# Performance work log

Measured on AMD Instinct MI355X. Metric: run time of the kernel, lower is better.

The kernel has to match this reference:

```python
import jax, jax.numpy as jnp
import numpy as np

N_NODES = 50000
N_EDGES = 800000
B, S, D = 512, 200, 128
H = 8


def setup_inputs() -> dict:
    key = jax.random.key(0)
    ks = iter(jax.random.split(key, 64))
    def nrm(shape, scale=0.05):
        return jax.random.normal(next(ks), shape, dtype=jnp.float32) * scale
    inp = {
        'hist_seq': jax.random.randint(next(ks), (B, S), 0, N_NODES, dtype=jnp.int32),
        'hist_answers': jax.random.randint(next(ks), (B, S), 0, 2, dtype=jnp.int32),
        'new_seq': jax.random.randint(next(ks), (B, S), 0, N_NODES, dtype=jnp.int32),
        'edge_index': jax.random.randint(next(ks), (2, N_EDGES), 0, N_NODES, dtype=jnp.int32),
        'node_x': nrm((N_NODES, D)),
        'gcn_w0': nrm((D, D)), 'gcn_b0': jnp.zeros((D,), jnp.float32),
        'gcn_w1': nrm((D, D)), 'gcn_b1': jnp.zeros((D,), jnp.float32),
        'gcn_w2': nrm((D, D)), 'gcn_b2': jnp.zeros((D,), jnp.float32),
        'ln0_g': jnp.ones((D,), jnp.float32), 'ln0_b': jnp.zeros((D,), jnp.float32),
        'ln1_g': jnp.ones((D,), jnp.float32), 'ln1_b': jnp.zeros((D,), jnp.float32),
        'ln2_g': jnp.ones((D,), jnp.float32), 'ln2_b': jnp.zeros((D,), jnp.float32),
        'ln3_g': jnp.ones((D,), jnp.float32), 'ln3_b': jnp.zeros((D,), jnp.float32),
        'corr_emb': nrm((2, D)),
        'lin0_w': nrm((2 * D, D)), 'lin0_b': jnp.zeros((D,), jnp.float32),
        'lin1_w': nrm((D, D)), 'lin2_w': nrm((D, D)), 'lin3_w': nrm((D, D)),
        'lin4_w': nrm((D, 1)), 'lin4_b': jnp.zeros((1,), jnp.float32),
        'pos_emb': nrm((S, D)),
        'mha_wq': nrm((D, D)), 'mha_bq': jnp.zeros((D,), jnp.float32),
        'mha_wk': nrm((D, D)), 'mha_bk': jnp.zeros((D,), jnp.float32),
        'mha_wv': nrm((D, D)), 'mha_bv': jnp.zeros((D,), jnp.float32),
        'mha_wo': nrm((D, D)), 'mha_bo': jnp.zeros((D,), jnp.float32),
        'ffn0_w': nrm((D, D)), 'ffn0_b': jnp.zeros((D,), jnp.float32),
        'ffn1_w': nrm((D, D)), 'ffn1_b': jnp.zeros((D,), jnp.float32),
    }
    return inp


def _layer_norm(x, g, b, eps=1e-5):
    m = jnp.mean(x, axis=-1, keepdims=True)
    v = jnp.var(x, axis=-1, keepdims=True)
    return (x - m) * jax.lax.rsqrt(v + eps) * g + b


def _forward(hist_seq, hist_answers, new_seq, edge_index, node_x,
             gcn_w0, gcn_b0, gcn_w1, gcn_b1, gcn_w2, gcn_b2,
             ln0_g, ln0_b, ln1_g, ln1_b, ln2_g, ln2_b, ln3_g, ln3_b,
             corr_emb, lin0_w, lin0_b, lin1_w, lin2_w, lin3_w, lin4_w, lin4_b,
             pos_emb, mha_wq, mha_bq, mha_wk, mha_bk, mha_wv, mha_bv,
             mha_wo, mha_bo, ffn0_w, ffn0_b, ffn1_w, ffn1_b):
    N = node_x.shape[0]
    loop = jnp.arange(N, dtype=edge_index.dtype)
    src = jnp.concatenate([edge_index[0], loop])  # self-loops as in PyG GCNConv
    dst = jnp.concatenate([edge_index[1], loop])
    deg = jax.ops.segment_sum(jnp.ones_like(dst, dtype=node_x.dtype), dst, num_segments=N)
    dis = jax.lax.rsqrt(deg)  # deg >= 1 (self-loops)
    norm = dis[src] * dis[dst]

    def gcn(x, W, b):
        xw = x @ W
        return jax.ops.segment_sum(norm[:, None] * xw[src], dst, num_segments=N) + b

    x = _layer_norm(jax.nn.relu(gcn(node_x, gcn_w0, gcn_b0)), ln0_g, ln0_b)
    x = _layer_norm(jax.nn.relu(gcn(x, gcn_w1, gcn_b1)), ln1_g, ln1_b)
    x = jax.nn.relu(gcn(x, gcn_w2, gcn_b2))  # last GCN layer: no LN

    # vectorized embedding gathers (the original's per-element loops)
    hist_emb = x[hist_seq]            # [B,S,D]
    new_emb = x[new_seq]              # [B,S,D]
    ans_emb = corr_emb[hist_answers]  # [B,S,D]

    inter = jnp.concatenate([hist_emb, ans_emb], axis=-1) @ lin0_w + lin0_b
    inter = inter + pos_emb[None]  # [B,S,D]

    v = inter @ lin1_w
    k = inter @ lin2_w
    q = new_emb @ lin3_w

    b_, s_, d_ = q.shape
    dh = d_ // H
    qh = (q @ mha_wq + mha_bq).reshape(b_, s_, H, dh)
    kh = (k @ mha_wk + mha_bk).reshape(b_, s_, H, dh)
    vh = (v @ mha_wv + mha_bv).reshape(b_, s_, H, dh)
    scores = jnp.einsum('bqhd,bkhd->bhqk', qh, kh) / jnp.sqrt(jnp.asarray(dh, q.dtype))
    causal = jnp.triu(jnp.ones((s_, s_), dtype=bool), k=1)
    scores = jnp.where(causal[None, None], -jnp.inf, scores)
    attn = jax.nn.softmax(scores, axis=-1)
    ao = jnp.einsum('bhqk,bkhd->bqhd', attn, vh).reshape(b_, s_, d_)
    ao = ao @ mha_wo + mha_bo

    atn = _layer_norm(ao + q, ln2_g, ln2_b)
    ffn = jax.nn.relu(atn @ ffn0_w + ffn0_b) @ ffn1_w + ffn1_b
    out = _layer_norm(ffn + atn, ln3_g, ln3_b)
    pred = (out @ lin4_w + lin4_b)[..., 0]  # squeeze -> [B,S]
    return pred


def reference(hist_seq, hist_answers, new_seq, edge_index, node_x,
              gcn_w0, gcn_b0, gcn_w1, gcn_b1, gcn_w2, gcn_b2,
              ln0_g, ln0_b, ln1_g, ln1_b, ln2_g, ln2_b, ln3_g, ln3_b,
              corr_emb, lin0_w, lin0_b, lin1_w, lin2_w, lin3_w, lin4_w, lin4_b,
              pos_emb, mha_wq, mha_bq, mha_wk, mha_bk, mha_wv, mha_bv,
              mha_wo, mha_bo, ffn0_w, ffn0_b, ffn1_w, ffn1_b):
    return _forward(hist_seq, hist_answers, new_seq, edge_index, node_x,
                    gcn_w0, gcn_b0, gcn_w1, gcn_b1, gcn_w2, gcn_b2,
                    ln0_g, ln0_b, ln1_g, ln1_b, ln2_g, ln2_b, ln3_g, ln3_b,
                    corr_emb, lin0_w, lin0_b, lin1_w, lin2_w, lin3_w, lin4_w, lin4_b,
                    pos_emb, mha_wq, mha_bq, mha_wk, mha_bk, mha_wv, mha_bv,
                    mha_wo, mha_bo, ffn0_w, ffn0_b, ffn1_w, ffn1_b)
```

## Files before the change

kernel.cpp:

```cpp
#include <hip/hip_runtime.h>
#include <math.h>

#define N_NODES 50000
#define N_EDGES 800000
#define B_ 512
#define S_ 200
#define D_ 128
#define BS_ (B_*S_)

typedef unsigned short u16;
typedef unsigned int u32;
using bfrag = __attribute__((ext_vector_type(8))) short;
using f32x4 = __attribute__((ext_vector_type(4))) float;
using i32x4 = __attribute__((ext_vector_type(4))) int;

__device__ __forceinline__ u16 f2bf(float f) {
  return (u16)((__float_as_uint(f) + 0x8000u) >> 16);
}
__device__ __forceinline__ float bf2f(u16 v) { return __uint_as_float(((u32)v) << 16); }
__device__ __forceinline__ float bflo(u32 v) { return __uint_as_float(v << 16); }
__device__ __forceinline__ float bfhi(u32 v) { return __uint_as_float(v & 0xffff0000u); }
__device__ __forceinline__ u32 pack2(float a, float b) {
  return (u32)f2bf(a) | ((u32)f2bf(b) << 16);
}
#define MFMA16(a, b, c) __builtin_amdgcn_mfma_f32_16x16x32_bf16((a), (b), (c), 0, 0, 0)

#define STAGE_W(Wsrc) \
  for (int i_ = threadIdx.x; i_ < 2048; i_ += 256) { \
    int c_ = i_ >> 4, kg_ = i_ & 15; \
    *(uint4*)(sW + c_ * 136 + kg_ * 8) = *(const uint4*)((Wsrc) + c_ * 128 + kg_ * 8); \
  }

__global__ void zero_i32_kernel(int* __restrict__ p, int n) {
  int i = blockIdx.x * 256 + threadIdx.x;
  if (i < n) p[i] = 0;
}

__global__ void f2bf8_kernel(const float* __restrict__ in, u16* __restrict__ out, int n8) {
  int i = blockIdx.x * 256 + threadIdx.x;
  if (i >= n8) return;
  float4 a = ((const float4*)in)[i * 2];
  float4 b = ((const float4*)in)[i * 2 + 1];
  uint4 o;
  o.x = pack2(a.x, a.y); o.y = pack2(a.z, a.w);
  o.z = pack2(b.x, b.y); o.w = pack2(b.z, b.w);
  ((uint4*)out)[i] = o;
}

__global__ __launch_bounds__(256) void wprep_kernel(
    const float* __restrict__ gcn_w0, const float* __restrict__ gcn_w1,
    const float* __restrict__ gcn_w2, const float* __restrict__ lin0_w,
    const float* __restrict__ lin3_w, const float* __restrict__ mha_wo,
    const float* __restrict__ ffn0_w, const float* __restrict__ ffn1_w,
    const float* __restrict__ lin1_w, const float* __restrict__ lin2_w,
    const float* __restrict__ mha_wq, const float* __restrict__ mha_wk,
    const float* __restrict__ mha_wv, const float* __restrict__ corr_emb,
    u16* __restrict__ g0T, u16* __restrict__ g1T, u16* __restrict__ g2T,
    u16* __restrict__ l0T, u16* __restrict__ l3T, u16* __restrict__ woT,
    u16* __restrict__ f0T, u16* __restrict__ f1T,
    u16* __restrict__ wqT, u16* __restrict__ wkT, u16* __restrict__ wvT,
    float* __restrict__ c01) {
  int bb = blockIdx.x;
  if (bb < 512) {
    const float* W; u16* D;
    switch (bb >> 6) {
      case 0: W = gcn_w0; D = g0T; break;
      case 1: W = gcn_w1; D = g1T; break;
      case 2: W = gcn_w2; D = g2T; break;
      case 3: W = lin0_w; D = l0T; break;
      case 4: W = lin3_w; D = l3T; break;
      case 5: W = mha_wo; D = woT; break;
      case 6: W = ffn0_w; D = f0T; break;
      default: W = ffn1_w; D = f1T; break;
    }
    int i = (bb & 63) * 256 + threadIdx.x;
    int k = i >> 7, c = i & 127;
    D[c * 128 + k] = f2bf(W[k * 128 + c]);
  } else if (bb < 704) {
    const float* X; const float* Y; u16* D;
    switch ((bb - 512) >> 6) {
      case 0: X = lin3_w; Y = mha_wq; D = wqT; break;
      case 1: X = lin2_w; Y = mha_wk; D = wkT; break;
      default: X = lin1_w; Y = mha_wv; D = wvT; break;
    }
    int i = ((bb - 512) & 63) * 256 + threadIdx.x;
    int k = i >> 7, c = i & 127;
    float acc = 0.f;
    for (int t = 0; t < 128; ++t) acc += X[k * 128 + t] * Y[t * 128 + c];
    D[c * 128 + k] = f2bf(acc);
  } else {
    int idx = threadIdx.x;
    int i = idx >> 7, j = idx & 127;
    float acc = 0.f;
    for (int t = 0; t < 128; ++t)
      acc += corr_emb[i * 128 + t] * lin0_w[128 * 128 + t * 128 + j];
    c01[idx] = acc;
  }
}

__global__ void pc_kernel(const float* __restrict__ lin0_b, const float* __restrict__ pos_emb,
                          const float* __restrict__ c01, float* __restrict__ pc) {
  int i = blockIdx.x * 256 + threadIdx.x;
  int c = i & 127, s = (i >> 7) % S_, a = i / (128 * S_);
  pc[i] = lin0_b[c] + pos_emb[s * 128 + c] + c01[a * 128 + c];
}

__global__ void hist_kernel(const int* __restrict__ dst, int* __restrict__ cnt, int E) {
  int e = blockIdx.x * 256 + threadIdx.x;
  if (e < E) atomicAdd(&cnt[dst[e]], 1);
}

__global__ __launch_bounds__(1024) void scanA_kernel(
    const int* __restrict__ cnt, int* __restrict__ locpref,
    int* __restrict__ btot, float* __restrict__ dis, int N) {
  __shared__ int wsum[16];
  int t = threadIdx.x, lane = t & 63, wid = t >> 6;
  int i = blockIdx.x * 1024 + t;
  int v = (i < N) ? cnt[i] : 0;
  if (i < N) dis[i] = rsqrtf(1.f + (float)v);
  int x = v;
  #pragma unroll
  for (int off = 1; off < 64; off <<= 1) {
    int y = __shfl_up(x, off);
    if (lane >= off) x += y;
  }
  if (lane == 63) wsum[wid] = x;
  __syncthreads();
  if (wid == 0 && lane < 16) {
    int s = wsum[lane];
    #pragma unroll
    for (int off = 1; off < 16; off <<= 1) {
      int y = __shfl_up(s, off);
      if (lane >= off) s += y;
    }
    wsum[lane] = s;
  }
  __syncthreads();
  int woff = (wid > 0) ? wsum[wid - 1] : 0;
  if (i < N) locpref[i] = woff + x - v;
  if (t == 1023) btot[blockIdx.x] = woff + x;
}

__global__ void scanB_kernel(const int* __restrict__ btot, int* __restrict__ boff, int nb) {
  int lane = threadIdx.x;
  int v = (lane < nb) ? btot[lane] : 0;
  int x = v;
  #pragma unroll
  for (int off = 1; off < 64; off <<= 1) {
    int y = __shfl_up(x, off);
    if (lane >= off) x += y;
  }
  if (lane < nb) boff[lane] = x - v;
}

__global__ void scanC_kernel(const int* __restrict__ locpref, const int* __restrict__ boff,
                             int* __restrict__ row_ptr, int* __restrict__ fill, int N) {
  int i = blockIdx.x * 256 + threadIdx.x;
  if (i < N) {
    int r = locpref[i] + boff[i >> 10];
    row_ptr[i] = r; fill[i] = r;
  }
  if (i == 0) row_ptr[N] = N_EDGES;
}

__global__ void scatter_kernel(const int* __restrict__ src, const int* __restrict__ dst,
                               int* __restrict__ fill, int* __restrict__ csr_src, int E) {
  int e = blockIdx.x * 256 + threadIdx.x;
  if (e >= E) return;
  int d = dst[e];
  int pos = atomicAdd(&fill[d], 1);
  csr_src[pos] = src[e];
}

__global__ __launch_bounds__(256) void gemm_bf16_kernel(
    const u16* __restrict__ A, const u16* __restrict__ wT,
    u16* __restrict__ C, int M) {
  __shared__ u16 ldsb[4][16 * 136];
  int t = threadIdx.x;
  int w = t >> 6, l = t & 63, lr = l & 15, lg = l >> 4;
  int r0 = blockIdx.x * 64 + w * 16;

  int row = r0 + lr;
  const u16* Arow = A + (size_t)(row < M ? row : 0) * 128;

  bfrag a[4];
  #pragma unroll
  for (int ks = 0; ks < 4; ++ks) a[ks] = *(const bfrag*)(Arow + ks * 32 + lg * 8);

  f32x4 acc[8];
  #pragma unroll
  for (int ct = 0; ct < 8; ++ct) acc[ct] = (f32x4){0.f, 0.f, 0.f, 0.f};
  #pragma unroll
  for (int ks = 0; ks < 4; ++ks)
    #pragma unroll
    for (int ct = 0; ct < 8; ++ct) {
      bfrag b = *(const bfrag*)(wT + (size_t)(ct * 16 + lr) * 128 + ks * 32 + lg * 8);
      acc[ct] = MFMA16(a[ks], b, acc[ct]);
    }
  #pragma unroll
  for (int ct = 0; ct < 8; ++ct)
    #pragma unroll
    for (int i = 0; i < 4; ++i)
      ldsb[w][(lg * 4 + i) * 136 + ct * 16 + lr] = f2bf(acc[ct][i]);
  #pragma unroll
  for (int j = 0; j < 4; ++j) {
    int c = j * 64 + l;
    int rw = c >> 4, ch = c & 15;
    int r = r0 + rw;
    if (r < M)
      *(uint4*)(C + (size_t)r * 128 + ch * 8) = *(const uint4*)&ldsb[w][rw * 136 + ch * 8];
  }
}

__global__ __launch_bounds__(256) void agg_kernel(
    const u16* __restrict__ xw, const float* __restrict__ dis,
    const int* __restrict__ row_ptr, const int* __restrict__ csr_src,
    const float* __restrict__ bias, const float* __restrict__ lng,
    const float* __restrict__ lnb, u16* __restrict__ out, int N, int doLN) {
  int t = threadIdx.x;
  int n = blockIdx.x * 4 + (t >> 6);
  if (n >= N) return;
  int l = t & 63, cg = l & 15, eg = l >> 4;
  float dn = dis[n];
  float acc[8] = {0.f, 0.f, 0.f, 0.f, 0.f, 0.f, 0.f, 0.f};
  if (eg == 0) {
    uint4 r = *(const uint4*)(xw + (size_t)n * 128 + cg * 8);
    float w = dn * dn;
    acc[0] += w * bflo(r.x); acc[1] += w * bfhi(r.x);
    acc[2] += w * bflo(r.y); acc[3] += w * bfhi(r.y);
    acc[4] += w * bflo(r.z); acc[5] += w * bfhi(r.z);
    acc[6] += w * bflo(r.w); acc[7] += w * bfhi(r.w);
  }
  int e1 = row_ptr[n + 1];
  int e = row_ptr[n] + eg;
  int sn = (e < e1) ? csr_src[e] : -1;
  while (sn >= 0) {
    int s = sn;
    e += 4;
    sn = (e < e1) ? csr_src[e] : -1;
    float w = dis[s] * dn;
    uint4 r = *(const uint4*)(xw + (size_t)s * 128 + cg * 8);
    acc[0] += w * bflo(r.x); acc[1] += w * bfhi(r.x);
    acc[2] += w * bflo(r.y); acc[3] += w * bfhi(r.y);
    acc[4] += w * bflo(r.z); acc[5] += w * bfhi(r.z);
    acc[6] += w * bflo(r.w); acc[7] += w * bfhi(r.w);
  }
  #pragma unroll
  for (int j = 0; j < 8; ++j) {
    acc[j] += __shfl_xor(acc[j], 16);
    acc[j] += __shfl_xor(acc[j], 32);
  }
  int c0 = cg * 8;
  #pragma unroll
  for (int j = 0; j < 8; ++j) acc[j] = fmaxf(acc[j] + bias[c0 + j], 0.f);
  if (doLN) {
    float s1 = 0.f, s2 = 0.f;
    #pragma unroll
    for (int j = 0; j < 8; ++j) { s1 += acc[j]; s2 += acc[j] * acc[j]; }
    #pragma unroll
    for (int off = 1; off < 16; off <<= 1) {
      s1 += __shfl_xor(s1, off);
      s2 += __shfl_xor(s2, off);
    }
    float mean = s1 * (1.f / 128.f);
    float var = s2 * (1.f / 128.f) - mean * mean;
    float inv = rsqrtf(var + 1e-5f);
    #pragma unroll
    for (int j = 0; j < 8; ++j)
      acc[j] = (acc[j] - mean) * inv * lng[c0 + j] + lnb[c0 + j];
  }
  if (eg == 0) {
    uint4 o;
    o.x = pack2(acc[0], acc[1]); o.y = pack2(acc[2], acc[3]);
    o.z = pack2(acc[4], acc[5]); o.w = pack2(acc[6], acc[7]);
    *(uint4*)(out + (size_t)n * 128 + cg * 8) = o;
  }
}

__global__ __launch_bounds__(256) void qkv_kernel(
    const u16* __restrict__ xa, const int* __restrict__ hist,
    const int* __restrict__ ans, const int* __restrict__ nseq,
    const u16* __restrict__ l0T, const float* __restrict__ pc,
    const u16* __restrict__ wkT, const float* __restrict__ bk,
    const u16* __restrict__ wvT, const float* __restrict__ bv,
    const u16* __restrict__ wqT, const float* __restrict__ bq,
    u16* __restrict__ khout, u16* __restrict__ vhout,
    u16* __restrict__ qhout, int nblk) {
  __shared__ u16 sW[128 * 136];
  __shared__ u16 ldsb[4][16 * 136];
  int bb = blockIdx.x;
  int t = threadIdx.x, w = t >> 6, l = t & 63, lr = l & 15, lg = l >> 4;
  f32x4 acc[8];

  if (bb < nblk) {
    int r0 = bb * 64 + w * 16;
    int arow = hist[r0 + lr];
    const u16* Arow = xa + (size_t)arow * 128;
    bfrag a[4];
    #pragma unroll
    for (int ks = 0; ks < 4; ++ks) a[ks] = *(const bfrag*)(Arow + ks * 32 + lg * 8);

    STAGE_W(l0T);
    __syncthreads();
    #pragma unroll
    for (int ct = 0; ct < 8; ++ct) acc[ct] = (f32x4){0.f, 0.f, 0.f, 0.f};
    #pragma unroll
    for (int ks = 0; ks < 4; ++ks)
      #pragma unroll
      for (int ct = 0; ct < 8; ++ct) {
        bfrag b = *(const bfrag*)(sW + (ct * 16 + lr) * 136 + ks * 32 + lg * 8);
        acc[ct] = MFMA16(a[ks], b, acc[ct]);
      }
    int pcoff[4];
    #pragma unroll
    for (int i = 0; i < 4; ++i) {
      int r = r0 + lg * 4 + i;
      pcoff[i] = (ans[r] * S_ + (r % S_)) * 128;
    }
    #pragma unroll
    for (int ct = 0; ct < 8; ++ct) {
      int col = ct * 16 + lr;
      #pragma unroll
      for (int i = 0; i < 4; ++i)
        ldsb[w][(lg * 4 + i) * 136 + col] = f2bf(acc[ct][i] + pc[pcoff[i] + col]);
    }
    bfrag a2[4];
    #pragma unroll
    for (int ks = 0; ks < 4; ++ks)
      a2[ks] = *(const bfrag*)(&ldsb[w][lr * 136 + ks * 32 + lg * 8]);
    __syncthreads();

    STAGE_W(wkT);
    __syncthreads();
    #pragma unroll
    for (int ct = 0; ct < 8; ++ct) acc[ct] = (f32x4){0.f, 0.f, 0.f, 0.f};
    #pragma unroll
    for (int ks = 0; ks < 4; ++ks)
      #pragma unroll
      for (int ct = 0; ct < 8; ++ct) {
        bfrag b = *(const bfrag*)(sW + (ct * 16 + lr) * 136 + ks * 32 + lg * 8);
        acc[ct] = MFMA16(a2[ks], b, acc[ct]);
      }
    #pragma unroll
    for (int ct = 0; ct < 8; ++ct)
      #pragma unroll
      for (int i = 0; i < 4; ++i)
        ldsb[w][(lg * 4 + i) * 136 + ct * 16 + lr] = f2bf(acc[ct][i] + bk[ct * 16 + lr]);
    #pragma unroll
    for (int j = 0; j < 4; ++j) {
      int c = j * 64 + l;
      int head = c >> 5, rw = (c >> 1) & 15, half = c & 1;
      *(uint4*)(khout + ((size_t)head * BS_ + r0 + rw) * 16 + half * 8) =
          *(const uint4*)&ldsb[w][rw * 136 + head * 16 + half * 8];
    }
    __syncthreads();

    STAGE_W(wvT);
    __syncthreads();
    #pragma unroll
    for (int ct = 0; ct < 8; ++ct) acc[ct] = (f32x4){0.f, 0.f, 0.f, 0.f};
    #pragma unroll
    for (int ks = 0; ks < 4; ++ks)
      #pragma unroll
      for (int ct = 0; ct < 8; ++ct) {
        bfrag b = *(const bfrag*)(sW + (ct * 16 + lr) * 136 + ks * 32 + lg * 8);
        acc[ct] = MFMA16(a2[ks], b, acc[ct]);
      }
    #pragma unroll
    for (int ct = 0; ct < 8; ++ct)
      #pragma unroll
      for (int i = 0; i < 4; ++i)
        ldsb[w][(lg * 4 + i) * 136 + ct * 16 + lr] = f2bf(acc[ct][i] + bv[ct * 16 + lr]);
    #pragma unroll
    for (int j = 0; j < 4; ++j) {
      int c = j * 64 + l;
      int head = c >> 5, rw = (c >> 1) & 15, half = c & 1;
      *(uint4*)(vhout + ((size_t)head * BS_ + r0 + rw) * 16 + half * 8) =
          *(const uint4*)&ldsb[w][rw * 136 + head * 16 + half * 8];
    }
  } else {
    int r0 = (bb - nblk) * 64 + w * 16;
    int arow = nseq[r0 + lr];
    const u16* Arow = xa + (size_t)arow * 128;
    bfrag a[4];
    #pragma unroll
    for (int ks = 0; ks < 4; ++ks) a[ks] = *(const bfrag*)(Arow + ks * 32 + lg * 8);

    STAGE_W(wqT);
    __syncthreads();
    #pragma unroll
    for (int ct = 0; ct < 8; ++ct) acc[ct] = (f32x4){0.f, 0.f, 0.f, 0.f};
    #pragma unroll
    for (int ks = 0; ks < 4; ++ks)
      #pragma unroll
      for (int ct = 0; ct < 8; ++ct) {
        bfrag b = *(const bfrag*)(sW + (ct * 16 + lr) * 136 + ks * 32 + lg * 8);
        acc[ct] = MFMA16(a[ks], b, acc[ct]);
      }
    #pragma unroll
    for (int ct = 0; ct < 8; ++ct)
      #pragma unroll
      for (int i = 0; i < 4; ++i)
        ldsb[w][(lg * 4 + i) * 136 + ct * 16 + lr] =
            f2bf((acc[ct][i] + bq[ct * 16 + lr]) * 0.25f);
    #pragma unroll
    for (int j = 0; j < 4; ++j) {
      int c = j * 64 + l;
      int head = c >> 5, rw = (c >> 1) & 15, half = c & 1;
      *(uint4*)(qhout + ((size_t)head * BS_ + r0 + rw) * 16 + half * 8) =
          *(const uint4*)&ldsb[w][rw * 136 + head * 16 + half * 8];
    }
  }
}

__global__ __launch_bounds__(256) void attn_mfma_kernel(
    u16* qh_ao, const u16* __restrict__ kh, const u16* __restrict__ vh) {
  __shared__ u16 Kl[208 * 24];
  __shared__ u16 Vt[16 * 232];
  int b = blockIdx.x >> 3, h = blockIdx.x & 7;
  int t = threadIdx.x;
  size_t base = ((size_t)h * BS_ + (size_t)b * S_) * 16;

  for (int i = t; i < 208 * 2; i += 256) {
    int key = i >> 1, d = (i & 1) * 8;
    uint4 v = make_uint4(0, 0, 0, 0);
    if (key < S_) v = *(const uint4*)(kh + base + (size_t)key * 16 + d);
    *(uint4*)(Kl + key * 24 + d) = v;
  }
  for (int i = t; i < 16 * 232; i += 256) {
    int d = i / 232, key = i - d * 232;
    Vt[d * 232 + key] = (key < S_) ? vh[base + (size_t)key * 16 + d] : (u16)0;
  }
  __syncthreads();

  int w = t >> 6, l = t & 63, lr = l & 15, lg = l >> 4;
  const f32x4 zero4 = {0.f, 0.f, 0.f, 0.f};
  const bfrag zerob = (bfrag){0, 0, 0, 0, 0, 0, 0, 0};
  u32 qpack = (w == 0) ? 0xFC71u : (w == 1) ? 0xFB80u : (w == 2) ? 0xFA92u : 0x6543u;
  int srcA = lr + ((lg & 1) << 5);
  int srcB = srcA + 16;
  bool hiTile = (lg >= 2);

  for (int s = 0; s < 4; ++s) {
    int qi = (qpack >> (4 * s)) & 15;
    if (qi == 15) break;
    int qrow = qi * 16 + lr;
    bfrag qf = zerob;
    if (lg < 2 && qrow < S_)
      qf = *(const bfrag*)(qh_ao + base + (size_t)qrow * 16 + lg * 8);
    float rsum = 0.f;
    f32x4 o = zero4;
    int ktmax = (qi + 2) >> 1;
    for (int kt = 0; kt < ktmax; ++kt) {
      int kj0 = kt * 2, kj1 = kt * 2 + 1;
      u32 P0t0, P1t0, P0t1 = 0, P1t1 = 0;
      {
        bfrag kf = zerob;
        if (lg < 2) kf = *(const bfrag*)(Kl + (kj0 * 16 + lr) * 24 + lg * 8);
        f32x4 sc = MFMA16(kf, qf, zero4);
        float p0, p1, p2, p3;
        if (kj0 == qi) {
          p0 = (lg * 4 + 0 <= lr) ? __expf(sc[0]) : 0.f;
          p1 = (lg * 4 + 1 <= lr) ? __expf(sc[1]) : 0.f;
          p2 = (lg * 4 + 2 <= lr) ? __expf(sc[2]) : 0.f;
          p3 = (lg * 4 + 3 <= lr) ? __expf(sc[3]) : 0.f;
        } else {
          p0 = __expf(sc[0]); p1 = __expf(sc[1]);
          p2 = __expf(sc[2]); p3 = __expf(sc[3]);
        }
        rsum += (p0 + p1) + (p2 + p3);
        P0t0 = pack2(p0, p1); P1t0 = pack2(p2, p3);
      }
      if (kj1 <= qi) {
        bfrag kf = zerob;
        if (lg < 2) kf = *(const bfrag*)(Kl + (kj1 * 16 + lr) * 24 + lg * 8);
        f32x4 sc = MFMA16(kf, qf, zero4);
        float p0, p1, p2, p3;
        if (kj1 == qi) {
          p0 = (lg * 4 + 0 <= lr) ? __expf(sc[0]) : 0.f;
          p1 = (lg * 4 + 1 <= lr) ? __expf(sc[1]) : 0.f;
          p2 = (lg * 4 + 2 <= lr) ? __expf(sc[2]) : 0.f;
          p3 = (lg * 4 + 3 <= lr) ? __expf(sc[3]) : 0.f;
        } else {
          p0 = __expf(sc[0]); p1 = __expf(sc[1]);
          p2 = __expf(sc[2]); p3 = __expf(sc[3]);
        }
        rsum += (p0 + p1) + (p2 + p3);
        P0t1 = pack2(p0, p1); P1t1 = pack2(p2, p3);
      }
      u32 x0 = __shfl(P0t0, srcA), x1 = __shfl(P1t0, srcA);
      u32 x2 = __shfl(P0t0, srcB), x3 = __shfl(P1t0, srcB);
      u32 y0 = __shfl(P0t1, srcA), y1 = __shfl(P1t1, srcA);
      u32 y2 = __shfl(P0t1, srcB), y3 = __shfl(P1t1, srcB);
      i32x4 pi;
      pi[0] = (int)(hiTile ? y0 : x0);
      pi[1] = (int)(hiTile ? y1 : x1);
      pi[2] = (int)(hiTile ? y2 : x2);
      pi[3] = (int)(hiTile ? y3 : x3);
      bfrag pb = __builtin_bit_cast(bfrag, pi);
      bfrag vf = *(const bfrag*)(Vt + lr * 232 + kt * 32 + lg * 8);
      o = MFMA16(vf, pb, o);
    }
    rsum += __shfl_xor(rsum, 16);
    rsum += __shfl_xor(rsum, 32);
    if (qrow < S_) {
      float inv = 1.f / rsum;
      uint2 ov;
      ov.x = pack2(o[0] * inv, o[1] * inv);
      ov.y = pack2(o[2] * inv, o[3] * inv);
      *(uint2*)(qh_ao + base + (size_t)qrow * 16 + lg * 4) = ov;
    }
  }
}

__global__ __launch_bounds__(256) void out_kernel(
    const u16* __restrict__ ao, const u16* __restrict__ xa,
    const int* __restrict__ nseq,
    const u16* __restrict__ woT, const float* __restrict__ bo,
    const u16* __restrict__ l3T,
    const float* __restrict__ g2, const float* __restrict__ b2,
    const u16* __restrict__ f0T, const float* __restrict__ b0f,
    const u16* __restrict__ f1T, const float* __restrict__ b1f,
    const float* __restrict__ g3, const float* __restrict__ b3,
    const float* __restrict__ w4, const float* __restrict__ b4,
    float* __restrict__ pred) {
  __shared__ u16 sW[128 * 136];
  __shared__ u16 ldsb[4][16 * 136];
  int t = threadIdx.x, w = t >> 6, l = t & 63, lr = l & 15, lg = l >> 4;
  int r0 = blockIdx.x * 64 + w * 16;

  bfrag a_ao[4], a_xa[4];
  #pragma unroll
  for (int ks = 0; ks < 4; ++ks) {
    int head = ks * 2 + (lg >> 1);
    int d0 = (lg & 1) * 8;
    a_ao[ks] = *(const bfrag*)(ao + ((size_t)head * BS_ + r0 + lr) * 16 + d0);
  }
  {
    int arow = nseq[r0 + lr];
    const u16* Arow = xa + (size_t)arow * 128;
    #pragma unroll
    for (int ks = 0; ks < 4; ++ks) a_xa[ks] = *(const bfrag*)(Arow + ks * 32 + lg * 8);
  }

  f32x4 acc[8];
  #pragma unroll
  for (int ct = 0; ct < 8; ++ct) acc[ct] = (f32x4){0.f, 0.f, 0.f, 0.f};

  STAGE_W(woT);
  __syncthreads();
  #pragma unroll
  for (int ks = 0; ks < 4; ++ks)
    #pragma unroll
    for (int ct = 0; ct < 8; ++ct) {
      bfrag b = *(const bfrag*)(sW + (ct * 16 + lr) * 136 + ks * 32 + lg * 8);
      acc[ct] = MFMA16(a_ao[ks], b, acc[ct]);
    }
  __syncthreads();

  STAGE_W(l3T);
  __syncthreads();
  #pragma unroll
  for (int ks = 0; ks < 4; ++ks)
    #pragma unroll
    for (int ct = 0; ct < 8; ++ct) {
      bfrag b = *(const bfrag*)(sW + (ct * 16 + lr) * 136 + ks * 32 + lg * 8);
      acc[ct] = MFMA16(a_xa[ks], b, acc[ct]);
    }
  __syncthreads();

  #pragma unroll
  for (int ct = 0; ct < 8; ++ct) {
    float bcol = bo[ct * 16 + lr];
    #pragma unroll
    for (int i = 0; i < 4; ++i) acc[ct][i] += bcol;
  }
  bfrag a2[4];
  {
    float s1[4] = {0, 0, 0, 0}, s2[4] = {0, 0, 0, 0};
    #pragma unroll
    for (int ct = 0; ct < 8; ++ct)
      #pragma unroll
      for (int i = 0; i < 4; ++i) {
        s1[i] += acc[ct][i];
        s2[i] += acc[ct][i] * acc[ct][i];
      }
    #pragma unroll
    for (int i = 0; i < 4; ++i) {
      s1[i] += __shfl_xor(s1[i], 1); s2[i] += __shfl_xor(s2[i], 1);
      s1[i] += __shfl_xor(s1[i], 2); s2[i] += __shfl_xor(s2[i], 2);
      s1[i] += __shfl_xor(s1[i], 4); s2[i] += __shfl_xor(s2[i], 4);
      s1[i] += __shfl_xor(s1[i], 8); s2[i] += __shfl_xor(s2[i], 8);
    }
    float mean[4], inv[4];
    #pragma unroll
    for (int i = 0; i < 4; ++i) {
      mean[i] = s1[i] * (1.f / 128.f);
      float var = s2[i] * (1.f / 128.f) - mean[i] * mean[i];
      inv[i] = rsqrtf(var + 1e-5f);
    }
    #pragma unroll
    for (int ct = 0; ct < 8; ++ct) {
      int col = ct * 16 + lr;
      float gc = g2[col], bc = b2[col];
      #pragma unroll
      for (int i = 0; i < 4; ++i) {
        acc[ct][i] = (acc[ct][i] - mean[i]) * inv[i] * gc + bc;
        ldsb[w][(lg * 4 + i) * 136 + col] = f2bf(acc[ct][i]);
      }
    }
    #pragma unroll
    for (int ks = 0; ks < 4; ++ks)
      a2[ks] = *(const bfrag*)(&ldsb[w][lr * 136 + ks * 32 + lg * 8]);
  }

  STAGE_W(f0T);
  __syncthreads();
  f32x4 acc2[8];
  #pragma unroll
  for (int ct = 0; ct < 8; ++ct) acc2[ct] = (f32x4){0.f, 0.f, 0.f, 0.f};
  #pragma unroll
  for (int ks = 0; ks < 4; ++ks)
    #pragma unroll
    for (int ct = 0; ct < 8; ++ct) {
      bfrag b = *(const bfrag*)(sW + (ct * 16 + lr) * 136 + ks * 32 + lg * 8);
      acc2[ct] = MFMA16(a2[ks], b, acc2[ct]);
    }
  #pragma unroll
  for (int ct = 0; ct < 8; ++ct) {
    int col = ct * 16 + lr;
    float bcol = b0f[col];
    #pragma unroll
    for (int i = 0; i < 4; ++i)
      ldsb[w][(lg * 4 + i) * 136 + col] = f2bf(fmaxf(acc2[ct][i] + bcol, 0.f));
  }
  #pragma unroll
  for (int ks = 0; ks < 4; ++ks)
    a2[ks] = *(const bfrag*)(&ldsb[w][lr * 136 + ks * 32 + lg * 8]);
  __syncthreads();

  STAGE_W(f1T);
  __syncthreads();
  #pragma unroll
  for (int ct = 0; ct < 8; ++ct) acc2[ct] = (f32x4){0.f, 0.f, 0.f, 0.f};
  #pragma unroll
  for (int ks = 0; ks < 4; ++ks)
    #pragma unroll
    for (int ct = 0; ct < 8; ++ct) {
      bfrag b = *(const bfrag*)(sW + (ct * 16 + lr) * 136 + ks * 32 + lg * 8);
      acc2[ct] = MFMA16(a2[ks], b, acc2[ct]);
    }
  #pragma unroll
  for (int ct = 0; ct < 8; ++ct) {
    int col = ct * 16 + lr;
    float bcol = b1f[col];
    #pragma unroll
    for (int i = 0; i < 4; ++i) acc2[ct][i] += bcol + acc[ct][i];
  }
  {
    float s1[4] = {0, 0, 0, 0}, s2[4] = {0, 0, 0, 0};
    #pragma unroll
    for (int ct = 0; ct < 8; ++ct)
      #pragma unroll
      for (int i = 0; i < 4; ++i) {
        s1[i] += acc2[ct][i];
        s2[i] += acc2[ct][i] * acc2[ct][i];
      }
    #pragma unroll
    for (int i = 0; i < 4; ++i) {
      s1[i] += __shfl_xor(s1[i], 1); s2[i] += __shfl_xor(s2[i], 1);
      s1[i] += __shfl_xor(s1[i], 2); s2[i] += __shfl_xor(s2[i], 2);
      s1[i] += __shfl_xor(s1[i], 4); s2[i] += __shfl_xor(s2[i], 4);
      s1[i] += __shfl_xor(s1[i], 8); s2[i] += __shfl_xor(s2[i], 8);
    }
    float p[4] = {0, 0, 0, 0};
    #pragma unroll
    for (int i = 0; i < 4; ++i) {
      float mean = s1[i] * (1.f / 128.f);
      float var = s2[i] * (1.f / 128.f) - mean * mean;
      float inv = rsqrtf(var + 1e-5f);
      #pragma unroll
      for (int ct = 0; ct < 8; ++ct) {
        int col = ct * 16 + lr;
        p[i] += ((acc2[ct][i] - mean) * inv * g3[col] + b3[col]) * w4[col];
      }
    }
    #pragma unroll
    for (int i = 0; i < 4; ++i) {
      p[i] += __shfl_xor(p[i], 1);
      p[i] += __shfl_xor(p[i], 2);
      p[i] += __shfl_xor(p[i], 4);
      p[i] += __shfl_xor(p[i], 8);
    }
    if (lr == 0) {
      float bias4 = b4[0];
      #pragma unroll
      for (int i = 0; i < 4; ++i) pred[r0 + lg * 4 + i] = p[i] + bias4;
    }
  }
}

extern "C" void kernel_launch(void* const* d_in, const int* in_sizes, int n_in,
                              void* d_out, int out_size, void* d_ws, size_t ws_size,
                              hipStream_t stream) {
  const int* hist_seq = (const int*)d_in[0];
  const int* hist_ans = (const int*)d_in[1];
  const int* new_seq = (const int*)d_in[2];
  const int* edge_index = (const int*)d_in[3];
  const float* node_x = (const float*)d_in[4];
  const float* gcn_w0 = (const float*)d_in[5];
  const float* gcn_b0 = (const float*)d_in[6];
  const float* gcn_w1 = (const float*)d_in[7];
  const float* gcn_b1 = (const float*)d_in[8];
  const float* gcn_w2 = (const float*)d_in[9];
  const float* gcn_b2 = (const float*)d_in[10];
  const float* ln0_g = (const float*)d_in[11];
  const float* ln0_b = (const float*)d_in[12];
  const float* ln1_g = (const float*)d_in[13];
  const float* ln1_b = (const float*)d_in[14];
  const float* ln2_g = (const float*)d_in[15];
  const float* ln2_b = (const float*)d_in[16];
  const float* ln3_g = (const float*)d_in[17];
  const float* ln3_b = (const float*)d_in[18];
  const float* corr_emb = (const float*)d_in[19];
  const float* lin0_w = (const float*)d_in[20];
  const float* lin0_b = (const float*)d_in[21];
  const float* lin1_w = (const float*)d_in[22];
  const float* lin2_w = (const float*)d_in[23];
  const float* lin3_w = (const float*)d_in[24];
  const float* lin4_w = (const float*)d_in[25];
  const float* lin4_b = (const float*)d_in[26];
  const float* pos_emb = (const float*)d_in[27];
  const float* mha_wq = (const float*)d_in[28];
  const float* mha_bq = (const float*)d_in[29];
  const float* mha_wk = (const float*)d_in[30];
  const float* mha_bk = (const float*)d_in[31];
  const float* mha_wv = (const float*)d_in[32];
  const float* mha_bv = (const float*)d_in[33];
  const float* mha_wo = (const float*)d_in[34];
  const float* mha_bo = (const float*)d_in[35];
  const float* ffn0_w = (const float*)d_in[36];
  const float* ffn0_b = (const float*)d_in[37];
  const float* ffn1_w = (const float*)d_in[38];
  const float* ffn1_b = (const float*)d_in[39];
  (void)in_sizes; (void)n_in; (void)out_size;

  char* ws = (char*)d_ws;
  size_t off = 0;
  auto alloc = [&](size_t bytes) -> void* {
    void* p = ws + off;
    off += (bytes + 255) & ~(size_t)255;
    return p;
  };
  int* cnt = (int*)alloc((size_t)N_NODES * 4);
  int* row_ptr = (int*)alloc((size_t)(N_NODES + 1) * 4);
  int* fill = (int*)alloc((size_t)N_NODES * 4);
  int* locpref = (int*)alloc((size_t)N_NODES * 4);
  int* btot = (int*)alloc(64 * 4);
  int* boff = (int*)alloc(64 * 4);
  float* dis = (float*)alloc((size_t)N_NODES * 4);
  int* csr_src = (int*)alloc((size_t)N_EDGES * 4);
  const size_t WB = 128 * 128 * 2;
  u16* g0T = (u16*)alloc(WB);
  u16* g1T = (u16*)alloc(WB);
  u16* g2T = (u16*)alloc(WB);
  u16* l0T = (u16*)alloc(WB);
  u16* l3T = (u16*)alloc(WB);
  u16* woT = (u16*)alloc(WB);
  u16* f0T = (u16*)alloc(WB);
  u16* f1T = (u16*)alloc(WB);
  u16* wqT = (u16*)alloc(WB);
  u16* wkT = (u16*)alloc(WB);
  u16* wvT = (u16*)alloc(WB);
  float* c01 = (float*)alloc(2 * 128 * 4);
  float* pc = (float*)alloc((size_t)2 * S_ * 128 * 4);
  u16* xa = (u16*)alloc((size_t)N_NODES * 128 * 2);
  const size_t CB = (size_t)BS_ * 128 * 2;
  size_t RB = off;
  u16* bufQ = (u16*)(ws + RB);
  u16* bufK = (u16*)(ws + RB + CB);
  u16* bufV = (u16*)(ws + RB + 2 * CB);
  u16* xb = bufQ;
  u16* xw = bufQ + (size_t)N_NODES * 128;
  size_t need = RB + 3 * CB;
  if (ws_size < need) return;

  int nb = (N_NODES + 1023) / 1024;
  zero_i32_kernel<<<(N_NODES + 255) / 256, 256, 0, stream>>>(cnt, N_NODES);
  hist_kernel<<<(N_EDGES + 255) / 256, 256, 0, stream>>>(edge_index + N_EDGES, cnt, N_EDGES);
  scanA_kernel<<<nb, 1024, 0, stream>>>(cnt, locpref, btot, dis, N_NODES);
  scanB_kernel<<<1, 64, 0, stream>>>(btot, boff, nb);
  scanC_kernel<<<(N_NODES + 255) / 256, 256, 0, stream>>>(locpref, boff, row_ptr, fill, N_NODES);
  scatter_kernel<<<(N_EDGES + 255) / 256, 256, 0, stream>>>(edge_index, edge_index + N_EDGES,
                                                            fill, csr_src, N_EDGES);
  wprep_kernel<<<705, 256, 0, stream>>>(gcn_w0, gcn_w1, gcn_w2, lin0_w, lin3_w, mha_wo,
                                        ffn0_w, ffn1_w, lin1_w, lin2_w, mha_wq, mha_wk,
                                        mha_wv, corr_emb, g0T, g1T, g2T, l0T, l3T, woT,
                                        f0T, f1T, wqT, wkT, wvT, c01);
  pc_kernel<<<(2 * S_ * 128 + 255) / 256, 256, 0, stream>>>(lin0_b, pos_emb, c01, pc);
  f2bf8_kernel<<<(N_NODES * 16 + 255) / 256, 256, 0, stream>>>(node_x, xb, N_NODES * 16);

  int gN = (N_NODES + 63) / 64;
  int aN = (N_NODES + 3) / 4;

  gemm_bf16_kernel<<<gN, 256, 0, stream>>>(xb, g0T, xw, N_NODES);
  agg_kernel<<<aN, 256, 0, stream>>>(xw, dis, row_ptr, csr_src, gcn_b0, ln0_g, ln0_b, xa, N_NODES, 1);
  gemm_bf16_kernel<<<gN, 256, 0, stream>>>(xa, g1T, xw, N_NODES);
  agg_kernel<<<aN, 256, 0, stream>>>(xw, dis, row_ptr, csr_src, gcn_b1, ln1_g, ln1_b, xa, N_NODES, 1);
  gemm_bf16_kernel<<<gN, 256, 0, stream>>>(xa, g2T, xw, N_NODES);
  agg_kernel<<<aN, 256, 0, stream>>>(xw, dis, row_ptr, csr_src, gcn_b2, nullptr, nullptr, xa, N_NODES, 0);

  int gT = BS_ / 64;
  qkv_kernel<<<2 * gT, 256, 0, stream>>>(xa, hist_seq, hist_ans, new_seq,
                                         l0T, pc, wkT, mha_bk, wvT, mha_bv,
                                         wqT, mha_bq, bufK, bufV, bufQ, gT);
  attn_mfma_kernel<<<B_ * 8, 256, 0, stream>>>(bufQ, bufK, bufV);
  out_kernel<<<gT, 256, 0, stream>>>(bufQ, xa, new_seq, woT, mha_bo, l3T,
                                     ln2_g, ln2_b, f0T, ffn0_b, f1T, ffn1_b,
                                     ln3_g, ln3_b, lin4_w, lin4_b, (float*)d_out);
}
```

Baseline: 417.3 us.

## Merge prep kernels, stage GCN weights in LDS, unroll edge aggregation by two

The separate zeroing, weight-transpose, positional-constant and node_x bf16 conversion kernels are folded into one prep_kernel launch, which cuts launch count and lets small jobs run alongside each other. The pc table is now computed directly, with each thread recomputing its corr_emb dot product. The GCN GEMM stages the transposed weight into shared memory instead of reading B fragments from global memory, at the cost of extra LDS and a barrier per block. The aggregation loop handles two neighbours per iteration so more gathers are in flight at once.

```diff
diff --git a/kernel.cpp b/kernel.cpp
--- a/kernel.cpp
+++ b/kernel.cpp
@@ -31,23 +31,8 @@
     *(uint4*)(sW + c_ * 136 + kg_ * 8) = *(const uint4*)((Wsrc) + c_ * 128 + kg_ * 8); \
   }
 
-__global__ void zero_i32_kernel(int* __restrict__ p, int n) {
-  int i = blockIdx.x * 256 + threadIdx.x;
-  if (i < n) p[i] = 0;
-}
-
-__global__ void f2bf8_kernel(const float* __restrict__ in, u16* __restrict__ out, int n8) {
-  int i = blockIdx.x * 256 + threadIdx.x;
-  if (i >= n8) return;
-  float4 a = ((const float4*)in)[i * 2];
-  float4 b = ((const float4*)in)[i * 2 + 1];
-  uint4 o;
-  o.x = pack2(a.x, a.y); o.y = pack2(a.z, a.w);
-  o.z = pack2(b.x, b.y); o.w = pack2(b.z, b.w);
-  ((uint4*)out)[i] = o;
-}
-
-__global__ __launch_bounds__(256) void wprep_kernel(
+__global__ __launch_bounds__(256) void prep_kernel(
+    int* __restrict__ cnt,
     const float* __restrict__ gcn_w0, const float* __restrict__ gcn_w1,
     const float* __restrict__ gcn_w2, const float* __restrict__ lin0_w,
     const float* __restrict__ lin3_w, const float* __restrict__ mha_wo,
@@ -55,15 +40,22 @@
     const float* __restrict__ lin1_w, const float* __restrict__ lin2_w,
     const float* __restrict__ mha_wq, const float* __restrict__ mha_wk,
     const float* __restrict__ mha_wv, const float* __restrict__ corr_emb,
+    const float* __restrict__ lin0_b, const float* __restrict__ pos_emb,
+    const float* __restrict__ node_x,
     u16* __restrict__ g0T, u16* __restrict__ g1T, u16* __restrict__ g2T,
     u16* __restrict__ l0T, u16* __restrict__ l3T, u16* __restrict__ woT,
     u16* __restrict__ f0T, u16* __restrict__ f1T,
     u16* __restrict__ wqT, u16* __restrict__ wkT, u16* __restrict__ wvT,
-    float* __restrict__ c01) {
+    float* __restrict__ pc, u16* __restrict__ xb) {
   int bb = blockIdx.x;
-  if (bb < 512) {
+  int t = threadIdx.x;
+  if (bb < 196) {
+    int i = bb * 256 + t;
+    if (i < N_NODES) cnt[i] = 0;
+  } else if (bb < 708) {
+    int idx = bb - 196;
     const float* W; u16* D;
-    switch (bb >> 6) {
+    switch (idx >> 6) {
       case 0: W = gcn_w0; D = g0T; break;
       case 1: W = gcn_w1; D = g1T; break;
       case 2: W = gcn_w2; D = g2T; break;
@@ -73,36 +65,40 @@
       case 6: W = ffn0_w; D = f0T; break;
       default: W = ffn1_w; D = f1T; break;
     }
-    int i = (bb & 63) * 256 + threadIdx.x;
+    int i = (idx & 63) * 256 + t;
     int k = i >> 7, c = i & 127;
     D[c * 128 + k] = f2bf(W[k * 128 + c]);
-  } else if (bb < 704) {
+  } else if (bb < 900) {
+    int idx = bb - 708;
     const float* X; const float* Y; u16* D;
-    switch ((bb - 512) >> 6) {
+    switch (idx >> 6) {
       case 0: X = lin3_w; Y = mha_wq; D = wqT; break;
       case 1: X = lin2_w; Y = mha_wk; D = wkT; break;
       default: X = lin1_w; Y = mha_wv; D = wvT; break;
     }
-    int i = ((bb - 512) & 63) * 256 + threadIdx.x;
+    int i = (idx & 63) * 256 + t;
     int k = i >> 7, c = i & 127;
     float acc = 0.f;
-    for (int t = 0; t < 128; ++t) acc += X[k * 128 + t] * Y[t * 128 + c];
+    for (int q = 0; q < 128; ++q) acc += X[k * 128 + q] * Y[q * 128 + c];
     D[c * 128 + k] = f2bf(acc);
+  } else if (bb < 1100) {
+    int i = (bb - 900) * 256 + t;
+    int c = i & 127, s = (i >> 7) % S_, a = i / (128 * S_);
+    float acc = lin0_b[c] + pos_emb[s * 128 + c];
+    for (int q = 0; q < 128; ++q)
+      acc += corr_emb[a * 128 + q] * lin0_w[(128 + q) * 128 + c];
+    pc[i] = acc;
   } else {
-    int idx = threadIdx.x;
-    int i = idx >> 7, j = idx & 127;
-    float acc = 0.f;
-    for (int t = 0; t < 128; ++t)
-      acc += corr_emb[i * 128 + t] * lin0_w[128 * 128 + t * 128 + j];
-    c01[idx] = acc;
-  }
-}
-
-__global__ void pc_kernel(const float* __restrict__ lin0_b, const float* __restrict__ pos_emb,
-                          const float* __restrict__ c01, float* __restrict__ pc) {
-  int i = blockIdx.x * 256 + threadIdx.x;
-  int c = i & 127, s = (i >> 7) % S_, a = i / (128 * S_);
-  pc[i] = lin0_b[c] + pos_emb[s * 128 + c] + c01[a * 128 + c];
+    int i = (bb - 1100) * 256 + t;
+    if (i < N_NODES * 16) {
+      float4 a4 = ((const float4*)node_x)[i * 2];
+      float4 b4 = ((const float4*)node_x)[i * 2 + 1];
+      uint4 o;
+      o.x = pack2(a4.x, a4.y); o.y = pack2(a4.z, a4.w);
+      o.z = pack2(b4.x, b4.y); o.w = pack2(b4.z, b4.w);
+      ((uint4*)xb)[i] = o;
+    }
+  }
 }
 
 __global__ void hist_kernel(const int* __restrict__ dst, int* __restrict__ cnt, int E) {
@@ -175,6 +171,7 @@
 __global__ __launch_bounds__(256) void gemm_bf16_kernel(
     const u16* __restrict__ A, const u16* __restrict__ wT,
     u16* __restrict__ C, int M) {
+  __shared__ u16 sW[128 * 136];
   __shared__ u16 ldsb[4][16 * 136];
   int t = threadIdx.x;
   int w = t >> 6, l = t & 63, lr = l & 15, lg = l >> 4;
@@ -187,6 +184,9 @@
   #pragma unroll
   for (int ks = 0; ks < 4; ++ks) a[ks] = *(const bfrag*)(Arow + ks * 32 + lg * 8);
 
+  STAGE_W(wT);
+  __syncthreads();
+
   f32x4 acc[8];
   #pragma unroll
   for (int ct = 0; ct < 8; ++ct) acc[ct] = (f32x4){0.f, 0.f, 0.f, 0.f};
@@ -194,7 +194,7 @@
   for (int ks = 0; ks < 4; ++ks)
     #pragma unroll
     for (int ct = 0; ct < 8; ++ct) {
-      bfrag b = *(const bfrag*)(wT + (size_t)(ct * 16 + lr) * 128 + ks * 32 + lg * 8);
+      bfrag b = *(const bfrag*)(sW + (ct * 16 + lr) * 136 + ks * 32 + lg * 8);
       acc[ct] = MFMA16(a[ks], b, acc[ct]);
     }
   #pragma unroll
@@ -233,17 +233,26 @@
   }
   int e1 = row_ptr[n + 1];
   int e = row_ptr[n] + eg;
-  int sn = (e < e1) ? csr_src[e] : -1;
-  while (sn >= 0) {
-    int s = sn;
-    e += 4;
-    sn = (e < e1) ? csr_src[e] : -1;
-    float w = dis[s] * dn;
-    uint4 r = *(const uint4*)(xw + (size_t)s * 128 + cg * 8);
-    acc[0] += w * bflo(r.x); acc[1] += w * bfhi(r.x);
-    acc[2] += w * bflo(r.y); acc[3] += w * bfhi(r.y);
-    acc[4] += w * bflo(r.z); acc[5] += w * bfhi(r.z);
-    acc[6] += w * bflo(r.w); acc[7] += w * bfhi(r.w);
+  int sn0 = (e < e1) ? csr_src[e] : -1;
+  int sn1 = (e + 4 < e1) ? csr_src[e + 4] : -1;
+  while (sn0 >= 0) {
+    int s0 = sn0;
+    int s1 = (sn1 >= 0) ? sn1 : sn0;
+    float w0 = dis[s0] * dn;
+    float w1 = (sn1 >= 0) ? dis[s1] * dn : 0.f;
+    e += 8;
+    sn0 = (e < e1) ? csr_src[e] : -1;
+    sn1 = (e + 4 < e1) ? csr_src[e + 4] : -1;
+    uint4 r0 = *(const uint4*)(xw + (size_t)s0 * 128 + cg * 8);
+    uint4 r1 = *(const uint4*)(xw + (size_t)s1 * 128 + cg * 8);
+    acc[0] += w0 * bflo(r0.x); acc[1] += w0 * bfhi(r0.x);
+    acc[2] += w0 * bflo(r0.y); acc[3] += w0 * bfhi(r0.y);
+    acc[4] += w0 * bflo(r0.z); acc[5] += w0 * bfhi(r0.z);
+    acc[6] += w0 * bflo(r0.w); acc[7] += w0 * bfhi(r0.w);
+    acc[0] += w1 * bflo(r1.x); acc[1] += w1 * bfhi(r1.x);
+    acc[2] += w1 * bflo(r1.y); acc[3] += w1 * bfhi(r1.y);
+    acc[4] += w1 * bflo(r1.z); acc[5] += w1 * bfhi(r1.z);
+    acc[6] += w1 * bflo(r1.w); acc[7] += w1 * bfhi(r1.w);
   }
   #pragma unroll
   for (int j = 0; j < 8; ++j) {
@@ -772,7 +781,6 @@
   u16* wqT = (u16*)alloc(WB);
   u16* wkT = (u16*)alloc(WB);
   u16* wvT = (u16*)alloc(WB);
-  float* c01 = (float*)alloc(2 * 128 * 4);
   float* pc = (float*)alloc((size_t)2 * S_ * 128 * 4);
   u16* xa = (u16*)alloc((size_t)N_NODES * 128 * 2);
   const size_t CB = (size_t)BS_ * 128 * 2;
@@ -785,20 +793,18 @@
   size_t need = RB + 3 * CB;
   if (ws_size < need) return;
 
+  prep_kernel<<<4225, 256, 0, stream>>>(cnt, gcn_w0, gcn_w1, gcn_w2, lin0_w, lin3_w,
+                                        mha_wo, ffn0_w, ffn1_w, lin1_w, lin2_w,
+                                        mha_wq, mha_wk, mha_wv, corr_emb, lin0_b,
+                                        pos_emb, node_x, g0T, g1T, g2T, l0T, l3T,
+                                        woT, f0T, f1T, wqT, wkT, wvT, pc, xb);
   int nb = (N_NODES + 1023) / 1024;
-  zero_i32_kernel<<<(N_NODES + 255) / 256, 256, 0, stream>>>(cnt, N_NODES);
   hist_kernel<<<(N_EDGES + 255) / 256, 256, 0, stream>>>(edge_index + N_EDGES, cnt, N_EDGES);
   scanA_kernel<<<nb, 1024, 0, stream>>>(cnt, locpref, btot, dis, N_NODES);
   scanB_kernel<<<1, 64, 0, stream>>>(btot, boff, nb);
   scanC_kernel<<<(N_NODES + 255) / 256, 256, 0, stream>>>(locpref, boff, row_ptr, fill, N_NODES);
   scatter_kernel<<<(N_EDGES + 255) / 256, 256, 0, stream>>>(edge_index, edge_index + N_EDGES,
                                                             fill, csr_src, N_EDGES);
-  wprep_kernel<<<705, 256, 0, stream>>>(gcn_w0, gcn_w1, gcn_w2, lin0_w, lin3_w, mha_wo,
-                                        ffn0_w, ffn1_w, lin1_w, lin2_w, mha_wq, mha_wk,
-                                        mha_wv, corr_emb, g0T, g1T, g2T, l0T, l3T, woT,
-                                        f0T, f1T, wqT, wkT, wvT, c01);
-  pc_kernel<<<(2 * S_ * 128 + 255) / 256, 256, 0, stream>>>(lin0_b, pos_emb, c01, pc);
-  f2bf8_kernel<<<(N_NODES * 16 + 255) / 256, 256, 0, stream>>>(node_x, xb, N_NODES * 16);
 
   int gN = (N_NODES + 63) / 64;
   int aN = (N_NODES + 3) / 4;
```

New measurement: 382.6 us. -8.3%, faster.
